# Performance work log

Measured on AMD Instinct MI355X. Metric: run time of the kernel, lower is better.

The kernel has to match this reference:

```python
import jax, jax.numpy as jnp
import numpy as np

N, T, C, O, K, L = 10000, 8, 16, 64, 16, 3


def setup_inputs():
    key = jax.random.key(0)
    ks = jax.random.split(key, 8)
    s = 0.05
    return dict(
        X=jax.random.normal(ks[0], (N, T, C), jnp.float32),
        As=jax.random.randint(ks[1], (L, T, N, K), 0, N, dtype=jnp.int32),
        key_out=jnp.zeros((1,), jnp.float32),
        key_states=jnp.zeros((2, 1), jnp.float32),
        conv_w=jax.random.normal(ks[2], (L, O, C), jnp.float32) * s,
        conv_b=jax.random.normal(ks[3], (L, O), jnp.float32) * s,
        W_ih=jax.random.normal(ks[4], (L, 4 * O, O), jnp.float32) * s,
        W_hh=jax.random.normal(ks[5], (L, 4 * O, O), jnp.float32) * s,
        b_ih=jax.random.normal(ks[6], (L, 4 * O), jnp.float32) * s,
        b_hh=jax.random.normal(ks[7], (L, 4 * O), jnp.float32) * s,
    )


def _lstm(seq, W_ih, W_hh, b_ih, b_hh):
    # seq: [T, N, O]; PyTorch LSTM gate order i, f, g, o; zero initial state.
    H = W_hh.shape[1]
    n = seq.shape[1]

    def step(carry, xt):
        h, c = carry
        gates = xt @ W_ih.T + h @ W_hh.T + (b_ih + b_hh)
        i, f, g, o = jnp.split(gates, 4, axis=-1)
        c = jax.nn.sigmoid(f) * c + jax.nn.sigmoid(i) * jnp.tanh(g)
        h = jax.nn.sigmoid(o) * jnp.tanh(c)
        return (h, c), h

    init = (jnp.zeros((n, H), seq.dtype), jnp.zeros((n, H), seq.dtype))
    (h, c), ys = jax.lax.scan(step, init, seq)
    return ys, h, c


def _level(x, A, conv_w, conv_b, W_ih, W_hh, b_ih, b_hh):
    # x: [N,T,C], A: [T,N,K] neighbor indices (align=1: ego-subtract)
    xt = jnp.transpose(x, (1, 0, 2))                       # [T,N,C]
    gathered = jax.vmap(lambda xtt, At: xtt[At])(xt, A)    # [T,N,K,C]
    rel = gathered - xt[:, :, None, :]                     # [T,N,K,C]
    # 1x1 conv over channel dim + bias
    feat = jnp.einsum('tnkc,oc->tnko', rel, conv_w) + conv_b  # [T,N,K,O]
    feat = feat.max(axis=2)                                # max-pool over K -> [T,N,O]
    ys, h, c = _lstm(feat, W_ih, W_hh, b_ih, b_hh)         # ys [T,N,O]
    return ys, h, c


def reference(X, As, key_out, key_states, conv_w, conv_b, W_ih, W_hh, b_ih, b_hh):
    # key_out/key_states only used by attention aggregator (type 5); unused here.
    ys, h, c = jax.vmap(_level, in_axes=(None, 0, 0, 0, 0, 0, 0, 0))(
        X, As, conv_w, conv_b, W_ih, W_hh, b_ih, b_hh)     # ys [L,T,N,O], h/c [L,N,O]
    # level_aggregate_type=1: AdaptiveMaxPool2d over the level axis = max over L
    X_out = jnp.transpose(ys.max(axis=0), (1, 0, 2))       # [N,T,O]
    state_h = h.max(axis=0)[:, None, :]                    # [N,1,O]
    state_c = c.max(axis=0)[:, None, :]                    # [N,1,O]
    return X_out, state_h, state_c
```

## Files before the change

### kernel.cpp

```cpp
#include <hip/hip_runtime.h>
#include <hip/hip_bf16.h>

#define NN 10000
#define TT 8
#define LL 3
#define NGRP 625

#define OUT_ELEMS 6400000
#define H_OFF 5120000
#define C_OFF 5760000

typedef __bf16 bf16;
typedef __attribute__((ext_vector_type(8))) __bf16 bf16x8;
typedef __attribute__((ext_vector_type(4))) float f32x4;
typedef __attribute__((ext_vector_type(16))) float f32x16;

__device__ __forceinline__ float sigf(float x) {
    return __builtin_amdgcn_rcpf(1.0f + __expf(-x));
}
__device__ __forceinline__ float tanhf_(float x) {
    return fmaf(2.0f, __builtin_amdgcn_rcpf(1.0f + __expf(-2.0f * x)), -1.0f);
}

__global__ void prep_kernel(const float* __restrict__ W_ih, const float* __restrict__ W_hh,
                            const float* __restrict__ b_ih, const float* __restrict__ b_hh,
                            bf16* __restrict__ wts, float* __restrict__ bias) {
    int id = blockIdx.x * 256 + threadIdx.x;
    if (id < LL * 2 * 256 * 64) {
        int col = id & 63;
        int row = (id >> 6) & 255;
        int mat = (id >> 14) & 1;
        int l = id >> 15;
        const float* src = mat ? W_hh : W_ih;
        float w = src[(l * 256 + row) * 64 + col];
        int kh = col >> 5, nt = row >> 4, nn = row & 15, kk = col & 31;
        wts[((((l * 2 + mat) * 2 + kh) * 16 + nt) * 16 + nn) * 32 + kk] = (bf16)w;
    } else {
        int id2 = id - LL * 2 * 256 * 64;
        if (id2 < LL * 256) bias[id2] = b_ih[id2] + b_hh[id2];
    }
}

__device__ __forceinline__ void level_body(
    int l, int node0, int tid,
    const float* __restrict__ X, const int* __restrict__ As,
    const float* __restrict__ conv_w, const float* __restrict__ conv_b,
    const bf16* __restrict__ wts, const float* __restrict__ bias,
    bf16 (*featL)[16][72], bf16 (*hlds)[16][72],
    float ymax[TT][4], float hfin[4], float cfin[4], bool accum) {
    const int lane = tid & 63;
    const int wv = tid >> 6;
    const int c16 = lane & 15;
    const int q = lane >> 4;
    const int m = lane & 31;
    const int hh = lane >> 5;
    const int ch0 = hh * 8;
    const int nsub = m >> 4;
    const int kn = m & 15;

    bf16x8 B0, B1;
    {
        const float* w0 = conv_w + ((l * 64 + m) * 16 + ch0);
        f32x4 a = *(const f32x4*)w0, b = *(const f32x4*)(w0 + 4);
        const float* w1 = conv_w + ((l * 64 + 32 + m) * 16 + ch0);
        f32x4 c = *(const f32x4*)w1, d = *(const f32x4*)(w1 + 4);
#pragma unroll
        for (int j = 0; j < 4; ++j) {
            B0[j] = (bf16)a[j]; B0[4 + j] = (bf16)b[j];
            B1[j] = (bf16)c[j]; B1[4 + j] = (bf16)d[j];
        }
    }
    const float cb0 = conv_b[l * 64 + m];
    const float cb1 = conv_b[l * 64 + 32 + m];

#pragma unroll 1
    for (int c = 0; c < 4; ++c) {
        const int pc = 2 * wv + (c & 1);
        const int t0 = (c >> 1) * 4;
        const int gn = node0 + 2 * pc + nsub;

        int aidx[4];
#pragma unroll
        for (int j = 0; j < 4; ++j)
            aidx[j] = As[((long)(l * 8 + t0 + j) * NN + gn) * 16 + kn];
        f32x4 sv[4][2], gv[4][2];
#pragma unroll
        for (int j = 0; j < 4; ++j) {
            const float* sp = X + ((gn * 8 + t0 + j) * 16 + ch0);
            sv[j][0] = *(const f32x4*)sp;
            sv[j][1] = *(const f32x4*)(sp + 4);
        }
#pragma unroll
        for (int j = 0; j < 4; ++j) {
            const float* gp = X + (((long)aidx[j] * 8 + t0 + j) * 16 + ch0);
            gv[j][0] = *(const f32x4*)gp;
            gv[j][1] = *(const f32x4*)(gp + 4);
        }

#pragma unroll
        for (int j = 0; j < 4; ++j) {
            bf16x8 af;
#pragma unroll
            for (int k = 0; k < 4; ++k) {
                af[k]     = (bf16)(gv[j][0][k] - sv[j][0][k]);
                af[4 + k] = (bf16)(gv[j][1][k] - sv[j][1][k]);
            }
            f32x16 D0, D1;
#pragma unroll
            for (int k = 0; k < 16; ++k) { D0[k] = 0.0f; D1[k] = 0.0f; }
            D0 = __builtin_amdgcn_mfma_f32_32x32x16_bf16(af, B0, D0, 0, 0, 0);
            D1 = __builtin_amdgcn_mfma_f32_32x32x16_bf16(af, B1, D1, 0, 0, 0);

            float v00 = D0[0], v01 = D1[0], v10 = D0[8], v11 = D1[8];
#pragma unroll
            for (int k = 1; k < 8; ++k) {
                v00 = fmaxf(v00, D0[k]);     v01 = fmaxf(v01, D1[k]);
                v10 = fmaxf(v10, D0[8 + k]); v11 = fmaxf(v11, D1[8 + k]);
            }
            v00 = fmaxf(v00, __shfl_xor(v00, 32));
            v01 = fmaxf(v01, __shfl_xor(v01, 32));
            v10 = fmaxf(v10, __shfl_xor(v10, 32));
            v11 = fmaxf(v11, __shfl_xor(v11, 32));

            const float sA = hh ? v10 : v00;
            const float sB = hh ? v11 : v01;
            featL[t0 + j][2 * pc + hh][m]      = (bf16)(sA + cb0);
            featL[t0 + j][2 * pc + hh][32 + m] = (bf16)(sB + cb1);
        }
    }

    const bf16* wb = wts + l * 32768;
    const int fo = c16 * 32 + q * 8;
    bf16x8 Bx0[4], Bx1[4], Bh0[4], Bh1[4];
    float brg[4];
#pragma unroll
    for (int g = 0; g < 4; ++g) {
        const int nt = 4 * g + wv;
        Bx0[g] = *(const bf16x8*)(wb + (0 * 16 + nt) * 512 + fo);
        Bx1[g] = *(const bf16x8*)(wb + (1 * 16 + nt) * 512 + fo);
        Bh0[g] = *(const bf16x8*)(wb + (2 * 16 + nt) * 512 + fo);
        Bh1[g] = *(const bf16x8*)(wb + (3 * 16 + nt) * 512 + fo);
        brg[g] = bias[l * 256 + nt * 16 + c16];
    }
    float c_r[4];
#pragma unroll
    for (int r = 0; r < 4; ++r) c_r[r] = 0.0f;

#pragma unroll
    for (int t = 0; t < TT; ++t) {
        __syncthreads();

        bf16x8 ax0 = *(const bf16x8*)&featL[t][c16][q * 8];
        bf16x8 ax1 = *(const bf16x8*)&featL[t][c16][32 + q * 8];
        bf16x8 ah0, ah1;
        if (t > 0) {
            ah0 = *(const bf16x8*)&hlds[(t + 1) & 1][c16][q * 8];
            ah1 = *(const bf16x8*)&hlds[(t + 1) & 1][c16][32 + q * 8];
        }

        f32x4 acc[4];
#pragma unroll
        for (int g = 0; g < 4; ++g) {
            float b = brg[g];
            acc[g] = (f32x4){b, b, b, b};
            acc[g] = __builtin_amdgcn_mfma_f32_16x16x32_bf16(ax0, Bx0[g], acc[g], 0, 0, 0);
            acc[g] = __builtin_amdgcn_mfma_f32_16x16x32_bf16(ax1, Bx1[g], acc[g], 0, 0, 0);
            if (t > 0) {
                acc[g] = __builtin_amdgcn_mfma_f32_16x16x32_bf16(ah0, Bh0[g], acc[g], 0, 0, 0);
                acc[g] = __builtin_amdgcn_mfma_f32_16x16x32_bf16(ah1, Bh1[g], acc[g], 0, 0, 0);
            }
        }

#pragma unroll
        for (int r = 0; r < 4; ++r) {
            float iv = acc[0][r], fv = acc[1][r], gg = acc[2][r], ov = acc[3][r];
            float c = sigf(fv) * c_r[r] + sigf(iv) * tanhf_(gg);
            c_r[r] = c;
            float h = sigf(ov) * tanhf_(c);
            hlds[t & 1][q * 4 + r][wv * 16 + c16] = (bf16)h;
            ymax[t][r] = accum ? fmaxf(ymax[t][r], h) : h;
            if (t == TT - 1) {
                hfin[r] = accum ? fmaxf(hfin[r], h) : h;
                cfin[r] = accum ? fmaxf(cfin[r], c) : c;
            }
        }
    }
}

__global__ __launch_bounds__(256, 3) void fused_split_kernel(
    const float* __restrict__ X, const int* __restrict__ As,
    const float* __restrict__ conv_w, const float* __restrict__ conv_b,
    const bf16* __restrict__ wts, const float* __restrict__ bias,
    float* __restrict__ slabs) {
    __shared__ __align__(16) bf16 featL[TT][16][72];
    __shared__ __align__(16) bf16 hlds[2][16][72];

    const int tid = threadIdx.x;
    const int l = blockIdx.x % 3;
    const int grp = blockIdx.x / 3;
    const int node0 = grp * 16;

    float ymax[TT][4], hfin[4], cfin[4];
    level_body(l, node0, tid, X, As, conv_w, conv_b, wts, bias,
               featL, hlds, ymax, hfin, cfin, false);

    float* slab = slabs + (long)l * OUT_ELEMS;
    const int lane = tid & 63;
    const int wv = tid >> 6;
    const int c16 = lane & 15;
    const int q = lane >> 4;
    const int col = wv * 16 + c16;
#pragma unroll
    for (int t = 0; t < TT; ++t)
#pragma unroll
        for (int r = 0; r < 4; ++r)
            slab[((long)(node0 + q * 4 + r) * 8 + t) * 64 + col] = ymax[t][r];
#pragma unroll
    for (int r = 0; r < 4; ++r) {
        slab[H_OFF + (long)(node0 + q * 4 + r) * 64 + col] = hfin[r];
        slab[C_OFF + (long)(node0 + q * 4 + r) * 64 + col] = cfin[r];
    }
}

__global__ __launch_bounds__(256) void reduce_kernel(
    const float* __restrict__ slabs, float* __restrict__ out) {
    const long i = (long)blockIdx.x * 256 + threadIdx.x;
    const f32x4* s0 = (const f32x4*)slabs;
    const f32x4* s1 = (const f32x4*)(slabs + OUT_ELEMS);
    const f32x4* s2 = (const f32x4*)(slabs + 2L * OUT_ELEMS);
    f32x4 a = s0[i], b = s1[i], c = s2[i], d;
#pragma unroll
    for (int k = 0; k < 4; ++k) d[k] = fmaxf(fmaxf(a[k], b[k]), c[k]);
    ((f32x4*)out)[i] = d;
}

__global__ __launch_bounds__(256, 3) void fused_kernel(
    const float* __restrict__ X, const int* __restrict__ As,
    const float* __restrict__ conv_w, const float* __restrict__ conv_b,
    const bf16* __restrict__ wts, const float* __restrict__ bias,
    float* __restrict__ out) {
    __shared__ __align__(16) bf16 featL[TT][16][72];
    __shared__ __align__(16) bf16 hlds[2][16][72];

    const int tid = threadIdx.x;
    const int node0 = blockIdx.x * 16;

    float ymax[TT][4], hfin[4], cfin[4];
    for (int l = 0; l < LL; ++l) {
        __syncthreads();
        level_body(l, node0, tid, X, As, conv_w, conv_b, wts, bias,
                   featL, hlds, ymax, hfin, cfin, (l > 0));
    }

    const int lane = tid & 63;
    const int wv = tid >> 6;
    const int c16 = lane & 15;
    const int q = lane >> 4;
    const int col = wv * 16 + c16;
#pragma unroll
    for (int t = 0; t < TT; ++t)
#pragma unroll
        for (int r = 0; r < 4; ++r)
            out[((long)(node0 + q * 4 + r) * 8 + t) * 64 + col] = ymax[t][r];
    float* sh = out + (long)H_OFF;
    float* sc = out + (long)C_OFF;
#pragma unroll
    for (int r = 0; r < 4; ++r) {
        sh[(long)(node0 + q * 4 + r) * 64 + col] = hfin[r];
        sc[(long)(node0 + q * 4 + r) * 64 + col] = cfin[r];
    }
}

extern "C" void kernel_launch(void* const* d_in, const int* in_sizes, int n_in,
                              void* d_out, int out_size, void* d_ws, size_t ws_size,
                              hipStream_t stream) {
    const float* X = (const float*)d_in[0];
    const int* As = (const int*)d_in[1];
    const float* conv_w = (const float*)d_in[4];
    const float* conv_b = (const float*)d_in[5];
    const float* W_ih = (const float*)d_in[6];
    const float* W_hh = (const float*)d_in[7];
    const float* b_ih = (const float*)d_in[8];
    const float* b_hh = (const float*)d_in[9];
    float* out = (float*)d_out;

    char* ws = (char*)d_ws;
    const size_t slabs_bytes = (size_t)3 * OUT_ELEMS * 4;
    const bool big_ws = ws_size >= slabs_bytes + 196608 + 4096;

    if (big_ws) {
        float* slabs = (float*)ws;
        bf16* wts = (bf16*)(ws + slabs_bytes);
        float* bias = (float*)(ws + slabs_bytes + 196608);
        hipLaunchKernelGGL(prep_kernel, dim3(387), dim3(256), 0, stream,
                           W_ih, W_hh, b_ih, b_hh, wts, bias);
        hipLaunchKernelGGL(fused_split_kernel, dim3(3 * NGRP), dim3(256), 0, stream,
                           X, As, conv_w, conv_b, wts, bias, slabs);
        hipLaunchKernelGGL(reduce_kernel, dim3(OUT_ELEMS / 4 / 256), dim3(256), 0, stream,
                           slabs, out);
    } else {
        bf16* wts = (bf16*)ws;
        float* bias = (float*)(ws + 196608);
        hipLaunchKernelGGL(prep_kernel, dim3(387), dim3(256), 0, stream,
                           W_ih, W_hh, b_ih, b_hh, wts, bias);
        hipLaunchKernelGGL(fused_kernel, dim3(NGRP), dim3(256), 0, stream,
                           X, As, conv_w, conv_b, wts, bias, out);
    }
}
```

Measured before the change: 167.8 us.

## Split conv/gather into a parallel kernel and run LSTM levels in one kernel

Replaces the per-level fused kernel plus the slab max-reduction with two stages. A highly parallel conv kernel, with one block per (level, timestep, node group), computes the gathered relative features and their max-pooled conv output, and writes them as bf16 to a workspace. An LSTM kernel then walks all three levels per node group, prefetching the next step's features and keeping the level max in registers. This removes the three fp32 output slabs and the reduce pass, at the cost of a bf16 feature round-trip through global memory and less parallelism in the recurrent stage (625 blocks).

```diff
diff --git a/kernel.cpp b/kernel.cpp
--- a/kernel.cpp
+++ b/kernel.cpp
@@ -9,6 +9,7 @@
 #define OUT_ELEMS 6400000
 #define H_OFF 5120000
 #define C_OFF 5760000
+#define FEAT_ELEMS (LL * TT * NN * 64)
 
 typedef __bf16 bf16;
 typedef __attribute__((ext_vector_type(8))) __bf16 bf16x8;
@@ -41,6 +42,198 @@
     }
 }
 
+__global__ __launch_bounds__(256, 4) void conv_kernel(
+    const float* __restrict__ X, const int* __restrict__ As,
+    const float* __restrict__ conv_w, const float* __restrict__ conv_b,
+    bf16* __restrict__ feat) {
+    const int bid = blockIdx.x;
+    const int t = bid & 7;
+    const int rest = bid >> 3;
+    const int l = rest / NGRP;
+    const int grp = rest - l * NGRP;
+    const int node0 = grp * 16;
+
+    const int tid = threadIdx.x;
+    const int lane = tid & 63;
+    const int wv = tid >> 6;
+    const int m = lane & 31;
+    const int hh = lane >> 5;
+    const int ch0 = hh * 8;
+    const int nsub = m >> 4;
+    const int kn = m & 15;
+
+    bf16x8 B0, B1;
+    {
+        const float* w0 = conv_w + ((l * 64 + m) * 16 + ch0);
+        f32x4 wa = *(const f32x4*)w0, wb = *(const f32x4*)(w0 + 4);
+        const float* w1 = conv_w + ((l * 64 + 32 + m) * 16 + ch0);
+        f32x4 wc = *(const f32x4*)w1, wd = *(const f32x4*)(w1 + 4);
+#pragma unroll
+        for (int j = 0; j < 4; ++j) {
+            B0[j] = (bf16)wa[j]; B0[4 + j] = (bf16)wb[j];
+            B1[j] = (bf16)wc[j]; B1[4 + j] = (bf16)wd[j];
+        }
+    }
+    const float cb0 = conv_b[l * 64 + m];
+    const float cb1 = conv_b[l * 64 + 32 + m];
+
+    int aidx[2];
+    f32x4 sv[2][2], gv[2][2];
+#pragma unroll
+    for (int it = 0; it < 2; ++it) {
+        const int p = 2 * wv + it;
+        const int gn = node0 + 2 * p + nsub;
+        aidx[it] = As[((long)(l * 8 + t) * NN + gn) * 16 + kn];
+        const float* sp = X + ((gn * 8 + t) * 16 + ch0);
+        sv[it][0] = *(const f32x4*)sp;
+        sv[it][1] = *(const f32x4*)(sp + 4);
+    }
+#pragma unroll
+    for (int it = 0; it < 2; ++it) {
+        const float* gp = X + (((long)aidx[it] * 8 + t) * 16 + ch0);
+        gv[it][0] = *(const f32x4*)gp;
+        gv[it][1] = *(const f32x4*)(gp + 4);
+    }
+#pragma unroll
+    for (int it = 0; it < 2; ++it) {
+        bf16x8 af;
+#pragma unroll
+        for (int k = 0; k < 4; ++k) {
+            af[k]     = (bf16)(gv[it][0][k] - sv[it][0][k]);
+            af[4 + k] = (bf16)(gv[it][1][k] - sv[it][1][k]);
+        }
+        f32x16 D0, D1;
+#pragma unroll
+        for (int k = 0; k < 16; ++k) { D0[k] = 0.0f; D1[k] = 0.0f; }
+        D0 = __builtin_amdgcn_mfma_f32_32x32x16_bf16(af, B0, D0, 0, 0, 0);
+        D1 = __builtin_amdgcn_mfma_f32_32x32x16_bf16(af, B1, D1, 0, 0, 0);
+
+        float v00 = D0[0], v01 = D1[0], v10 = D0[8], v11 = D1[8];
+#pragma unroll
+        for (int k = 1; k < 8; ++k) {
+            v00 = fmaxf(v00, D0[k]);     v01 = fmaxf(v01, D1[k]);
+            v10 = fmaxf(v10, D0[8 + k]); v11 = fmaxf(v11, D1[8 + k]);
+        }
+        v00 = fmaxf(v00, __shfl_xor(v00, 32));
+        v01 = fmaxf(v01, __shfl_xor(v01, 32));
+        v10 = fmaxf(v10, __shfl_xor(v10, 32));
+        v11 = fmaxf(v11, __shfl_xor(v11, 32));
+
+        const float sA = hh ? v10 : v00;
+        const float sB = hh ? v11 : v01;
+        const int p = 2 * wv + it;
+        const int n = node0 + 2 * p + hh;
+        bf16* fp = feat + ((long)(l * 8 + t) * NN + n) * 64;
+        fp[m]      = (bf16)(sA + cb0);
+        fp[32 + m] = (bf16)(sB + cb1);
+    }
+}
+
+__global__ __launch_bounds__(256, 3) void lstm_kernel(
+    const bf16* __restrict__ feat, const bf16* __restrict__ wts,
+    const float* __restrict__ bias, float* __restrict__ out) {
+    __shared__ __align__(16) bf16 hlds[2][16][72];
+
+    const int tid = threadIdx.x;
+    const int node0 = blockIdx.x * 16;
+    const int lane = tid & 63;
+    const int wv = tid >> 6;
+    const int c16 = lane & 15;
+    const int q = lane >> 4;
+
+    float ymax[TT][4], hfin[4], cfin[4];
+#pragma unroll
+    for (int t = 0; t < TT; ++t)
+#pragma unroll
+        for (int r = 0; r < 4; ++r) ymax[t][r] = -1e30f;
+#pragma unroll
+    for (int r = 0; r < 4; ++r) { hfin[r] = -1e30f; cfin[r] = -1e30f; }
+
+    const bf16* fbase = feat + (long)(node0 + c16) * 64 + q * 8;
+    bf16x8 pax0 = *(const bf16x8*)fbase;
+    bf16x8 pax1 = *(const bf16x8*)(fbase + 32);
+
+#pragma unroll 1
+    for (int l = 0; l < LL; ++l) {
+        const bf16* wb = wts + l * 32768;
+        const int fo = c16 * 32 + q * 8;
+        bf16x8 Bx0[4], Bx1[4], Bh0[4], Bh1[4];
+        float brg[4];
+#pragma unroll
+        for (int g = 0; g < 4; ++g) {
+            const int nt = 4 * g + wv;
+            Bx0[g] = *(const bf16x8*)(wb + (0 * 16 + nt) * 512 + fo);
+            Bx1[g] = *(const bf16x8*)(wb + (1 * 16 + nt) * 512 + fo);
+            Bh0[g] = *(const bf16x8*)(wb + (2 * 16 + nt) * 512 + fo);
+            Bh1[g] = *(const bf16x8*)(wb + (3 * 16 + nt) * 512 + fo);
+            brg[g] = bias[l * 256 + nt * 16 + c16];
+        }
+        float c_r[4];
+#pragma unroll
+        for (int r = 0; r < 4; ++r) c_r[r] = 0.0f;
+
+#pragma unroll
+        for (int t = 0; t < TT; ++t) {
+            __syncthreads();
+
+            bf16x8 ax0 = pax0, ax1 = pax1;
+            const int ltn = l * 8 + t + 1;
+            if (ltn < LL * TT) {
+                const bf16* fp = fbase + (long)ltn * (NN * 64);
+                pax0 = *(const bf16x8*)fp;
+                pax1 = *(const bf16x8*)(fp + 32);
+            }
+
+            bf16x8 ah0, ah1;
+            if (t > 0) {
+                ah0 = *(const bf16x8*)&hlds[(t + 1) & 1][c16][q * 8];
+                ah1 = *(const bf16x8*)&hlds[(t + 1) & 1][c16][32 + q * 8];
+            }
+
+            f32x4 acc[4];
+#pragma unroll
+            for (int g = 0; g < 4; ++g) {
+                const float bb = brg[g];
+                acc[g] = (f32x4){bb, bb, bb, bb};
+                acc[g] = __builtin_amdgcn_mfma_f32_16x16x32_bf16(ax0, Bx0[g], acc[g], 0, 0, 0);
+                acc[g] = __builtin_amdgcn_mfma_f32_16x16x32_bf16(ax1, Bx1[g], acc[g], 0, 0, 0);
+                if (t > 0) {
+                    acc[g] = __builtin_amdgcn_mfma_f32_16x16x32_bf16(ah0, Bh0[g], acc[g], 0, 0, 0);
+                    acc[g] = __builtin_amdgcn_mfma_f32_16x16x32_bf16(ah1, Bh1[g], acc[g], 0, 0, 0);
+                }
+            }
+
+#pragma unroll
+            for (int r = 0; r < 4; ++r) {
+                float iv = acc[0][r], fv = acc[1][r], gg = acc[2][r], ov = acc[3][r];
+                float c = sigf(fv) * c_r[r] + sigf(iv) * tanhf_(gg);
+                c_r[r] = c;
+                float h = sigf(ov) * tanhf_(c);
+                hlds[t & 1][q * 4 + r][wv * 16 + c16] = (bf16)h;
+                ymax[t][r] = fmaxf(ymax[t][r], h);
+                if (t == TT - 1) {
+                    hfin[r] = fmaxf(hfin[r], h);
+                    cfin[r] = fmaxf(cfin[r], c);
+                }
+            }
+        }
+    }
+
+    const int col = wv * 16 + c16;
+#pragma unroll
+    for (int t = 0; t < TT; ++t)
+#pragma unroll
+        for (int r = 0; r < 4; ++r)
+            out[((long)(node0 + q * 4 + r) * 8 + t) * 64 + col] = ymax[t][r];
+    float* sh = out + (long)H_OFF;
+    float* sc = out + (long)C_OFF;
+#pragma unroll
+    for (int r = 0; r < 4; ++r) {
+        sh[(long)(node0 + q * 4 + r) * 64 + col] = hfin[r];
+        sc[(long)(node0 + q * 4 + r) * 64 + col] = cfin[r];
+    }
+}
+
 __device__ __forceinline__ void level_body(
     int l, int node0, int tid,
     const float* __restrict__ X, const int* __restrict__ As,
@@ -187,53 +380,6 @@
     }
 }
 
-__global__ __launch_bounds__(256, 3) void fused_split_kernel(
-    const float* __restrict__ X, const int* __restrict__ As,
-    const float* __restrict__ conv_w, const float* __restrict__ conv_b,
-    const bf16* __restrict__ wts, const float* __restrict__ bias,
-    float* __restrict__ slabs) {
-    __shared__ __align__(16) bf16 featL[TT][16][72];
-    __shared__ __align__(16) bf16 hlds[2][16][72];
-
-    const int tid = threadIdx.x;
-    const int l = blockIdx.x % 3;
-    const int grp = blockIdx.x / 3;
-    const int node0 = grp * 16;
-
-    float ymax[TT][4], hfin[4], cfin[4];
-    level_body(l, node0, tid, X, As, conv_w, conv_b, wts, bias,
-               featL, hlds, ymax, hfin, cfin, false);
-
-    float* slab = slabs + (long)l * OUT_ELEMS;
-    const int lane = tid & 63;
-    const int wv = tid >> 6;
-    const int c16 = lane & 15;
-    const int q = lane >> 4;
-    const int col = wv * 16 + c16;
-#pragma unroll
-    for (int t = 0; t < TT; ++t)
-#pragma unroll
-        for (int r = 0; r < 4; ++r)
-            slab[((long)(node0 + q * 4 + r) * 8 + t) * 64 + col] = ymax[t][r];
-#pragma unroll
-    for (int r = 0; r < 4; ++r) {
-        slab[H_OFF + (long)(node0 + q * 4 + r) * 64 + col] = hfin[r];
-        slab[C_OFF + (long)(node0 + q * 4 + r) * 64 + col] = cfin[r];
-    }
-}
-
-__global__ __launch_bounds__(256) void reduce_kernel(
-    const float* __restrict__ slabs, float* __restrict__ out) {
-    const long i = (long)blockIdx.x * 256 + threadIdx.x;
-    const f32x4* s0 = (const f32x4*)slabs;
-    const f32x4* s1 = (const f32x4*)(slabs + OUT_ELEMS);
-    const f32x4* s2 = (const f32x4*)(slabs + 2L * OUT_ELEMS);
-    f32x4 a = s0[i], b = s1[i], c = s2[i], d;
-#pragma unroll
-    for (int k = 0; k < 4; ++k) d[k] = fmaxf(fmaxf(a[k], b[k]), c[k]);
-    ((f32x4*)out)[i] = d;
-}
-
 __global__ __launch_bounds__(256, 3) void fused_kernel(
     const float* __restrict__ X, const int* __restrict__ As,
     const float* __restrict__ conv_w, const float* __restrict__ conv_b,
@@ -285,19 +431,19 @@
     float* out = (float*)d_out;
 
     char* ws = (char*)d_ws;
-    const size_t slabs_bytes = (size_t)3 * OUT_ELEMS * 4;
-    const bool big_ws = ws_size >= slabs_bytes + 196608 + 4096;
+    const size_t feat_bytes = (size_t)FEAT_ELEMS * 2;
+    const bool big_ws = ws_size >= feat_bytes + 196608 + 4096;
 
     if (big_ws) {
-        float* slabs = (float*)ws;
-        bf16* wts = (bf16*)(ws + slabs_bytes);
-        float* bias = (float*)(ws + slabs_bytes + 196608);
+        bf16* feat = (bf16*)ws;
+        bf16* wts = (bf16*)(ws + feat_bytes);
+        float* bias = (float*)(ws + feat_bytes + 196608);
         hipLaunchKernelGGL(prep_kernel, dim3(387), dim3(256), 0, stream,
                            W_ih, W_hh, b_ih, b_hh, wts, bias);
-        hipLaunchKernelGGL(fused_split_kernel, dim3(3 * NGRP), dim3(256), 0, stream,
-                           X, As, conv_w, conv_b, wts, bias, slabs);
-        hipLaunchKernelGGL(reduce_kernel, dim3(OUT_ELEMS / 4 / 256), dim3(256), 0, stream,
-                           slabs, out);
+        hipLaunchKernelGGL(conv_kernel, dim3(8 * LL * NGRP), dim3(256), 0, stream,
+                           X, As, conv_w, conv_b, feat);
+        hipLaunchKernelGGL(lstm_kernel, dim3(NGRP), dim3(256), 0, stream,
+                           feat, wts, bias, out);
     } else {
         bf16* wts = (bf16*)ws;
         float* bias = (float*)(ws + 196608);
```

Result: slower. 206.1 us (+22.9%).

## Stream per-step LSTM outputs through LDS for coalesced slab stores

Applied to the files above, without the earlier changes.

Adds a new per-level split kernel that writes each timestep's h into a float LDS buffer and stores the previous step's tile as coalesced 16-byte rows to the slab inside the time loop. This replaces keeping all eight timesteps' outputs in registers and issuing scattered 4-byte stores at the end. Register pressure drops, launch bounds move to 4 blocks per SM, and global writes overlap with the recurrence. The cost is an extra LDS buffer and LDS traffic each step; the final h and c are also routed through LDS.

```diff
diff --git a/kernel.cpp b/kernel.cpp
--- a/kernel.cpp
+++ b/kernel.cpp
@@ -41,6 +41,191 @@
     }
 }
 
+__global__ __launch_bounds__(256, 4) void fused_split2_kernel(
+    const float* __restrict__ X, const int* __restrict__ As,
+    const float* __restrict__ conv_w, const float* __restrict__ conv_b,
+    const bf16* __restrict__ wts, const float* __restrict__ bias,
+    float* __restrict__ slabs) {
+    __shared__ __align__(16) bf16 featL[TT][16][72];
+    __shared__ __align__(16) bf16 hlds[2][16][72];
+    __shared__ __align__(16) float ylds[2][16][64];
+
+    const int tid = threadIdx.x;
+    const int l = blockIdx.x % 3;
+    const int grp = blockIdx.x / 3;
+    const int node0 = grp * 16;
+
+    const int lane = tid & 63;
+    const int wv = tid >> 6;
+    const int c16 = lane & 15;
+    const int q = lane >> 4;
+    const int m = lane & 31;
+    const int hh = lane >> 5;
+    const int ch0 = hh * 8;
+    const int nsub = m >> 4;
+    const int kn = m & 15;
+
+    bf16x8 B0, B1;
+    {
+        const float* w0 = conv_w + ((l * 64 + m) * 16 + ch0);
+        f32x4 a = *(const f32x4*)w0, b = *(const f32x4*)(w0 + 4);
+        const float* w1 = conv_w + ((l * 64 + 32 + m) * 16 + ch0);
+        f32x4 c = *(const f32x4*)w1, d = *(const f32x4*)(w1 + 4);
+#pragma unroll
+        for (int j = 0; j < 4; ++j) {
+            B0[j] = (bf16)a[j]; B0[4 + j] = (bf16)b[j];
+            B1[j] = (bf16)c[j]; B1[4 + j] = (bf16)d[j];
+        }
+    }
+    const float cb0 = conv_b[l * 64 + m];
+    const float cb1 = conv_b[l * 64 + 32 + m];
+
+#pragma unroll 1
+    for (int c = 0; c < 4; ++c) {
+        const int pc = 2 * wv + (c & 1);
+        const int t0 = (c >> 1) * 4;
+        const int gn = node0 + 2 * pc + nsub;
+
+        int aidx[4];
+#pragma unroll
+        for (int j = 0; j < 4; ++j)
+            aidx[j] = As[((long)(l * 8 + t0 + j) * NN + gn) * 16 + kn];
+        f32x4 sv[4][2], gv[4][2];
+#pragma unroll
+        for (int j = 0; j < 4; ++j) {
+            const float* sp = X + ((gn * 8 + t0 + j) * 16 + ch0);
+            sv[j][0] = *(const f32x4*)sp;
+            sv[j][1] = *(const f32x4*)(sp + 4);
+        }
+#pragma unroll
+        for (int j = 0; j < 4; ++j) {
+            const float* gp = X + (((long)aidx[j] * 8 + t0 + j) * 16 + ch0);
+            gv[j][0] = *(const f32x4*)gp;
+            gv[j][1] = *(const f32x4*)(gp + 4);
+        }
+
+#pragma unroll
+        for (int j = 0; j < 4; ++j) {
+            bf16x8 af;
+#pragma unroll
+            for (int k = 0; k < 4; ++k) {
+                af[k]     = (bf16)(gv[j][0][k] - sv[j][0][k]);
+                af[4 + k] = (bf16)(gv[j][1][k] - sv[j][1][k]);
+            }
+            f32x16 D0, D1;
+#pragma unroll
+            for (int k = 0; k < 16; ++k) { D0[k] = 0.0f; D1[k] = 0.0f; }
+            D0 = __builtin_amdgcn_mfma_f32_32x32x16_bf16(af, B0, D0, 0, 0, 0);
+            D1 = __builtin_amdgcn_mfma_f32_32x32x16_bf16(af, B1, D1, 0, 0, 0);
+
+            float v00 = D0[0], v01 = D1[0], v10 = D0[8], v11 = D1[8];
+#pragma unroll
+            for (int k = 1; k < 8; ++k) {
+                v00 = fmaxf(v00, D0[k]);     v01 = fmaxf(v01, D1[k]);
+                v10 = fmaxf(v10, D0[8 + k]); v11 = fmaxf(v11, D1[8 + k]);
+            }
+            v00 = fmaxf(v00, __shfl_xor(v00, 32));
+            v01 = fmaxf(v01, __shfl_xor(v01, 32));
+            v10 = fmaxf(v10, __shfl_xor(v10, 32));
+            v11 = fmaxf(v11, __shfl_xor(v11, 32));
+
+            const float sA = hh ? v10 : v00;
+            const float sB = hh ? v11 : v01;
+            featL[t0 + j][2 * pc + hh][m]      = (bf16)(sA + cb0);
+            featL[t0 + j][2 * pc + hh][32 + m] = (bf16)(sB + cb1);
+        }
+    }
+
+    const bf16* wb = wts + l * 32768;
+    const int fo = c16 * 32 + q * 8;
+    bf16x8 Bx0[4], Bx1[4], Bh0[4], Bh1[4];
+    float brg[4];
+#pragma unroll
+    for (int g = 0; g < 4; ++g) {
+        const int nt = 4 * g + wv;
+        Bx0[g] = *(const bf16x8*)(wb + (0 * 16 + nt) * 512 + fo);
+        Bx1[g] = *(const bf16x8*)(wb + (1 * 16 + nt) * 512 + fo);
+        Bh0[g] = *(const bf16x8*)(wb + (2 * 16 + nt) * 512 + fo);
+        Bh1[g] = *(const bf16x8*)(wb + (3 * 16 + nt) * 512 + fo);
+        brg[g] = bias[l * 256 + nt * 16 + c16];
+    }
+    float c_r[4];
+#pragma unroll
+    for (int r = 0; r < 4; ++r) c_r[r] = 0.0f;
+
+    const int sn = tid >> 4;
+    const int sc = (tid & 15) * 4;
+    float* slab = slabs + (long)l * OUT_ELEMS;
+
+#pragma unroll
+    for (int t = 0; t < TT; ++t) {
+        __syncthreads();
+
+        if (t > 0) {
+            f32x4 yv = *(const f32x4*)&ylds[(t - 1) & 1][sn][sc];
+            *(f32x4*)&slab[((long)(node0 + sn) * 8 + (t - 1)) * 64 + sc] = yv;
+        }
+
+        bf16x8 ax0 = *(const bf16x8*)&featL[t][c16][q * 8];
+        bf16x8 ax1 = *(const bf16x8*)&featL[t][c16][32 + q * 8];
+        bf16x8 ah0, ah1;
+        if (t > 0) {
+            ah0 = *(const bf16x8*)&hlds[(t + 1) & 1][c16][q * 8];
+            ah1 = *(const bf16x8*)&hlds[(t + 1) & 1][c16][32 + q * 8];
+        }
+
+        f32x4 acc[4];
+#pragma unroll
+        for (int g = 0; g < 4; ++g) {
+            float b = brg[g];
+            acc[g] = (f32x4){b, b, b, b};
+            acc[g] = __builtin_amdgcn_mfma_f32_16x16x32_bf16(ax0, Bx0[g], acc[g], 0, 0, 0);
+            acc[g] = __builtin_amdgcn_mfma_f32_16x16x32_bf16(ax1, Bx1[g], acc[g], 0, 0, 0);
+            if (t > 0) {
+                acc[g] = __builtin_amdgcn_mfma_f32_16x16x32_bf16(ah0, Bh0[g], acc[g], 0, 0, 0);
+                acc[g] = __builtin_amdgcn_mfma_f32_16x16x32_bf16(ah1, Bh1[g], acc[g], 0, 0, 0);
+            }
+        }
+
+#pragma unroll
+        for (int r = 0; r < 4; ++r) {
+            float iv = acc[0][r], fv = acc[1][r], gg = acc[2][r], ov = acc[3][r];
+            float c = sigf(fv) * c_r[r] + sigf(iv) * tanhf_(gg);
+            c_r[r] = c;
+            float h = sigf(ov) * tanhf_(c);
+            hlds[t & 1][q * 4 + r][wv * 16 + c16] = (bf16)h;
+            ylds[t & 1][q * 4 + r][wv * 16 + c16] = h;
+        }
+    }
+
+    __syncthreads();
+    {
+        f32x4 yv = *(const f32x4*)&ylds[1][sn][sc];
+        *(f32x4*)&slab[((long)(node0 + sn) * 8 + 7) * 64 + sc] = yv;
+        *(f32x4*)&slab[H_OFF + (long)(node0 + sn) * 64 + sc] = yv;
+    }
+#pragma unroll
+    for (int r = 0; r < 4; ++r)
+        ylds[0][q * 4 + r][wv * 16 + c16] = c_r[r];
+    __syncthreads();
+    {
+        f32x4 cv = *(const f32x4*)&ylds[0][sn][sc];
+        *(f32x4*)&slab[C_OFF + (long)(node0 + sn) * 64 + sc] = cv;
+    }
+}
+
+__global__ __launch_bounds__(256) void reduce_kernel(
+    const float* __restrict__ slabs, float* __restrict__ out) {
+    const long i = (long)blockIdx.x * 256 + threadIdx.x;
+    const f32x4* s0 = (const f32x4*)slabs;
+    const f32x4* s1 = (const f32x4*)(slabs + OUT_ELEMS);
+    const f32x4* s2 = (const f32x4*)(slabs + 2L * OUT_ELEMS);
+    f32x4 a = s0[i], b = s1[i], c = s2[i], d;
+#pragma unroll
+    for (int k = 0; k < 4; ++k) d[k] = fmaxf(fmaxf(a[k], b[k]), c[k]);
+    ((f32x4*)out)[i] = d;
+}
+
 __device__ __forceinline__ void level_body(
     int l, int node0, int tid,
     const float* __restrict__ X, const int* __restrict__ As,
@@ -187,53 +372,6 @@
     }
 }
 
-__global__ __launch_bounds__(256, 3) void fused_split_kernel(
-    const float* __restrict__ X, const int* __restrict__ As,
-    const float* __restrict__ conv_w, const float* __restrict__ conv_b,
-    const bf16* __restrict__ wts, const float* __restrict__ bias,
-    float* __restrict__ slabs) {
-    __shared__ __align__(16) bf16 featL[TT][16][72];
-    __shared__ __align__(16) bf16 hlds[2][16][72];
-
-    const int tid = threadIdx.x;
-    const int l = blockIdx.x % 3;
-    const int grp = blockIdx.x / 3;
-    const int node0 = grp * 16;
-
-    float ymax[TT][4], hfin[4], cfin[4];
-    level_body(l, node0, tid, X, As, conv_w, conv_b, wts, bias,
-               featL, hlds, ymax, hfin, cfin, false);
-
-    float* slab = slabs + (long)l * OUT_ELEMS;
-    const int lane = tid & 63;
-    const int wv = tid >> 6;
-    const int c16 = lane & 15;
-    const int q = lane >> 4;
-    const int col = wv * 16 + c16;
-#pragma unroll
-    for (int t = 0; t < TT; ++t)
-#pragma unroll
-        for (int r = 0; r < 4; ++r)
-            slab[((long)(node0 + q * 4 + r) * 8 + t) * 64 + col] = ymax[t][r];
-#pragma unroll
-    for (int r = 0; r < 4; ++r) {
-        slab[H_OFF + (long)(node0 + q * 4 + r) * 64 + col] = hfin[r];
-        slab[C_OFF + (long)(node0 + q * 4 + r) * 64 + col] = cfin[r];
-    }
-}
-
-__global__ __launch_bounds__(256) void reduce_kernel(
-    const float* __restrict__ slabs, float* __restrict__ out) {
-    const long i = (long)blockIdx.x * 256 + threadIdx.x;
-    const f32x4* s0 = (const f32x4*)slabs;
-    const f32x4* s1 = (const f32x4*)(slabs + OUT_ELEMS);
-    const f32x4* s2 = (const f32x4*)(slabs + 2L * OUT_ELEMS);
-    f32x4 a = s0[i], b = s1[i], c = s2[i], d;
-#pragma unroll
-    for (int k = 0; k < 4; ++k) d[k] = fmaxf(fmaxf(a[k], b[k]), c[k]);
-    ((f32x4*)out)[i] = d;
-}
-
 __global__ __launch_bounds__(256, 3) void fused_kernel(
     const float* __restrict__ X, const int* __restrict__ As,
     const float* __restrict__ conv_w, const float* __restrict__ conv_b,
@@ -294,7 +432,7 @@
         float* bias = (float*)(ws + slabs_bytes + 196608);
         hipLaunchKernelGGL(prep_kernel, dim3(387), dim3(256), 0, stream,
                            W_ih, W_hh, b_ih, b_hh, wts, bias);
-        hipLaunchKernelGGL(fused_split_kernel, dim3(3 * NGRP), dim3(256), 0, stream,
+        hipLaunchKernelGGL(fused_split2_kernel, dim3(3 * NGRP), dim3(256), 0, stream,
                            X, As, conv_w, conv_b, wts, bias, slabs);
         hipLaunchKernelGGL(reduce_kernel, dim3(OUT_ELEMS / 4 / 256), dim3(256), 0, stream,
                            slabs, out);
```

New measurement: 159.5 us. 1.05x faster.
